# Optimization experiments

Hardware: AMD Instinct MI355X
Metric: run time of the kernel (lower is better)

The kernel has to match this reference:

```python
import jax, jax.numpy as jnp
import numpy as np

B = 32          # num graphs
N = 4096        # nodes per graph (temporal length after reshape)
TOT = B * N     # 131072 total nodes
F = 64          # num_features
HS = 128        # hidden_dim_s
RS = 32         # rank_s
HT = 128        # hidden_dim_t
RT = 32         # rank_t
E = 1048576     # num edges


def setup_inputs() -> dict:
    key = jax.random.key(0)
    ks = jax.random.split(key, 20)
    x = jax.random.normal(ks[0], (TOT, F), jnp.float32)
    edge_index = jax.random.randint(ks[1], (2, E), 0, TOT, dtype=jnp.int64)
    batch = jnp.repeat(jnp.arange(B, dtype=jnp.int64), N)

    def lin(k, fan_in, fan_out):
        s = 1.0 / np.sqrt(fan_in)
        return jax.random.uniform(k, (fan_in, fan_out), jnp.float32, -s, s)

    def conv(k, cout, cin):
        s = 1.0 / np.sqrt(cin * 3)
        return jax.random.uniform(k, (cout, cin, 3), jnp.float32, -s, s)

    return {
        "x": x, "edge_index": edge_index, "batch": batch,
        "W1": lin(ks[2], F, HS), "b1": jnp.zeros((HS,), jnp.float32),
        "W2": lin(ks[3], HS, RS), "b2": jnp.zeros((RS,), jnp.float32),
        "W3": lin(ks[4], RS, HS), "b3": jnp.zeros((HS,), jnp.float32),
        "tW1": conv(ks[5], HT, HS), "tb1": jnp.zeros((HT,), jnp.float32),
        "tW2": conv(ks[6], RT, HT), "tb2": jnp.zeros((RT,), jnp.float32),
        "tW3": conv(ks[7], HT, RT), "tb3": jnp.zeros((HT,), jnp.float32),
        "Wpi": lin(ks[8], HT, 1), "bpi": jnp.zeros((1,), jnp.float32),
        "Wn": lin(ks[9], HT, 1), "bn": jnp.zeros((1,), jnp.float32),
        "Wp": lin(ks[10], HT, 1), "bp": jnp.zeros((1,), jnp.float32),
    }


def reference(x, edge_index, batch,
              W1, b1, W2, b2, W3, b3,
              tW1, tb1, tW2, tb2, tW3, tb3,
              Wpi, bpi, Wn, bn, Wp, bp):
    src, dst = edge_index[0], edge_index[1]
    n = x.shape[0]

    # GCN symmetric normalization with added self-loops (PyG GCNConv default)
    deg = jnp.zeros((n,), x.dtype).at[dst].add(1.0) + 1.0  # +1 self-loop
    dinv = jax.lax.rsqrt(deg)
    enorm = dinv[src] * dinv[dst]       # [E] edge normalization
    snorm = dinv * dinv                 # [n] self-loop normalization

    def gcn(h, W, b):
        h = h @ W                                            # [n, out]
        agg = jnp.zeros_like(h).at[dst].add(h[src] * enorm[:, None])
        return agg + h * snorm[:, None] + b

    xs = jax.nn.relu(gcn(x, W1, b1))
    xs = jax.nn.relu(gcn(xs, W2, b2))
    xs = jax.nn.relu(gcn(xs, W3, b3))    # [TOT, HS]

    num_graphs = B  # == batch.max() + 1 (batch is repeat(arange(B), N))
    xs = xs.reshape(num_graphs, -1, xs.shape[-1]).transpose(0, 2, 1)  # [B, HS, N]

    def conv1d(z, w, bias):
        y = jax.lax.conv_general_dilated(
            z, w, window_strides=(1,), padding=((1, 1),),
            dimension_numbers=("NCH", "OIH", "NCH"))
        return y + bias[None, :, None]

    xt = jax.nn.relu(conv1d(xs, tW1, tb1))
    xt = jax.nn.relu(conv1d(xt, tW2, tb2))
    xt = jax.nn.relu(conv1d(xt, tW3, tb3))                   # [B, HT, N]

    xt = xt.transpose(0, 2, 1).reshape(-1, xt.shape[1])      # [TOT, HT]

    pi = jax.nn.sigmoid(xt @ Wpi + bpi)
    nb = jax.nn.softplus(xt @ Wn + bn)
    p = jax.nn.sigmoid(xt @ Wp + bp)
    return (pi, nb, p)
```

## Files before the change

kernel.cpp:

```cpp
#include <hip/hip_runtime.h>
#include <cmath>

constexpr int TOT = 131072;
constexpr int NE  = 1048576;
constexpr int NMASK = 4095;

constexpr int NB   = 512;
constexpr int DPB  = 256;
constexpr int BCAP = 4096;
constexpr int EPB  = 2048;

typedef __attribute__((ext_vector_type(8))) short bf16x8;
typedef __attribute__((ext_vector_type(4))) float f32x4;

__device__ inline float bf2f(unsigned int u16) {
    union { unsigned int i; float f; } x; x.i = u16 << 16; return x.f;
}
__device__ inline unsigned short f2bf(float f) {
    union { float f; unsigned int i; } x; x.f = f;
    unsigned int r = (x.i + 0x7fffu + ((x.i >> 16) & 1u)) >> 16;
    return (unsigned short)r;
}
__device__ inline void unpack8(uint4 v, float* f) {
    f[0] = bf2f(v.x & 0xffffu); f[1] = bf2f(v.x >> 16);
    f[2] = bf2f(v.y & 0xffffu); f[3] = bf2f(v.y >> 16);
    f[4] = bf2f(v.z & 0xffffu); f[5] = bf2f(v.z >> 16);
    f[6] = bf2f(v.w & 0xffffu); f[7] = bf2f(v.w >> 16);
}
__device__ inline uint4 pack8(const float* f) {
    uint4 v;
    v.x = (unsigned)f2bf(f[0]) | ((unsigned)f2bf(f[1]) << 16);
    v.y = (unsigned)f2bf(f[2]) | ((unsigned)f2bf(f[3]) << 16);
    v.z = (unsigned)f2bf(f[4]) | ((unsigned)f2bf(f[5]) << 16);
    v.w = (unsigned)f2bf(f[6]) | ((unsigned)f2bf(f[7]) << 16);
    return v;
}

__global__ __launch_bounds__(256) void k_part(const int* __restrict__ src,
                                              const int* __restrict__ dst,
                                              int* __restrict__ gcur,
                                              unsigned* __restrict__ buf) {
    __shared__ int hist[NB];
    __shared__ int cbase[NB];
    __shared__ int lcur[NB];
    const int tid = threadIdx.x;
    const int e0 = blockIdx.x * EPB;

    for (int b = tid; b < NB; b += 256) hist[b] = 0;
    __syncthreads();
    for (int i = tid; i < EPB; i += 256)
        atomicAdd(&hist[dst[e0 + i] >> 8], 1);
    __syncthreads();
    for (int b = tid; b < NB; b += 256) {
        int c = hist[b];
        cbase[b] = (c > 0) ? atomicAdd(&gcur[b * 32], c) : 0;
        lcur[b] = 0;
    }
    __syncthreads();
    for (int i = tid; i < EPB; i += 256) {
        int e = e0 + i;
        int d = dst[e];
        int b = d >> 8;
        int p = atomicAdd(&lcur[b], 1);
        buf[b * BCAP + cbase[b] + p] = ((unsigned)src[e] << 8) | (unsigned)(d & 255);
    }
}

__global__ __launch_bounds__(256) void k_bcsr(const unsigned* __restrict__ buf,
                                              const int* __restrict__ gcur,
                                              int* __restrict__ adj,
                                              int2* __restrict__ rse,
                                              float* __restrict__ dinv,
                                              const float4* __restrict__ x,
                                              uint4* __restrict__ xsc) {
    __shared__ int cnt[DPB];
    __shared__ int start[DPB];
    __shared__ int cur[DPB];
    __shared__ int sc[DPB];
    const int b = blockIdx.x;
    const int tid = threadIdx.x;
    cnt[tid] = 0;
    __syncthreads();
    const int n = gcur[b * 32];
    const unsigned* eb = buf + b * BCAP;
    for (int i = tid; i < n; i += 256)
        atomicAdd(&cnt[eb[i] & 255u], 1);
    __syncthreads();
    int v = cnt[tid];
    sc[tid] = v;
    __syncthreads();
    for (int off = 1; off < 256; off <<= 1) {
        int a = sc[tid];
        int p = (tid >= off) ? sc[tid - off] : 0;
        __syncthreads();
        sc[tid] = a + p;
        __syncthreads();
    }
    int st = sc[tid] - v;
    start[tid] = st;
    cur[tid] = 0;
    int d = (b << 8) + tid;
    rse[d] = make_int2(b * BCAP + st, v);
    dinv[d] = rsqrtf((float)v + 1.0f);
    __syncthreads();
    for (int i = tid; i < n; i += 256) {
        unsigned w = eb[i];
        int dl = (int)(w & 255u);
        int p = atomicAdd(&cur[dl], 1);
        adj[b * BCAP + start[dl] + p] = (int)(w >> 8);
    }
    for (int i = tid; i < DPB * 8; i += 256) {
        int rl = i >> 3;
        int t = (b << 11) + i;
        float dv = rsqrtf((float)cnt[rl] + 1.0f);
        float4 v0 = x[t * 2], v1 = x[t * 2 + 1];
        float f[8] = { v0.x * dv, v0.y * dv, v0.z * dv, v0.w * dv,
                       v1.x * dv, v1.y * dv, v1.z * dv, v1.w * dv };
        xsc[t] = pack8(f);
    }
}

__global__ __launch_bounds__(256) void k_packall(
    const float* __restrict__ W1, const float* __restrict__ W2, const float* __restrict__ W3,
    const float* __restrict__ tW1, const float* __restrict__ tW2, const float* __restrict__ tW3,
    unsigned short* __restrict__ g1, unsigned short* __restrict__ g2, unsigned short* __restrict__ g3,
    unsigned short* __restrict__ c1, unsigned short* __restrict__ c2, unsigned short* __restrict__ c3) {
    int gid = blockIdx.x * 256 + threadIdx.x;
    const float* w; unsigned short* wp; int CIN, COUT, taps, idx;
    if      (gid <  8192) { w = W1;  wp = g1; CIN = 64;  COUT = 128; taps = 1; idx = gid; }
    else if (gid < 12288) { w = W2;  wp = g2; CIN = 128; COUT = 32;  taps = 1; idx = gid - 8192; }
    else if (gid < 16384) { w = W3;  wp = g3; CIN = 32;  COUT = 128; taps = 1; idx = gid - 12288; }
    else if (gid < 65536) { w = tW1; wp = c1; CIN = 128; COUT = 128; taps = 3; idx = gid - 16384; }
    else if (gid < 77824) { w = tW2; wp = c2; CIN = 128; COUT = 32;  taps = 3; idx = gid - 65536; }
    else if (gid < 90112) { w = tW3; wp = c3; CIN = 32;  COUT = 128; taps = 3; idx = gid - 77824; }
    else return;
    int j = idx & 7;
    int L = (idx >> 3) & 63;
    int f = idx >> 9;
    int NT = COUT >> 4;
    int kc = f / NT, nt = f - kc * NT;
    int k = kc * 32 + (L >> 4) * 8 + j;
    int n = nt * 16 + (L & 15);
    float v;
    if (taps == 1) v = w[k * COUT + n];
    else { int t = k / CIN, c = k - t * CIN; v = w[(n * CIN + c) * 3 + t]; }
    wp[idx] = f2bf(v);
}

template<int LC>
__global__ __launch_bounds__(256) void k_gcsr(const uint4* __restrict__ xs,
                                              const int* __restrict__ adj,
                                              const int2* __restrict__ rse,
                                              const float* __restrict__ dinv,
                                              const float* __restrict__ bias,
                                              uint4* __restrict__ out) {
    int t = blockIdx.x * 256 + threadIdx.x;
    int d = t >> LC;
    int g = t & ((1 << LC) - 1);
    float a[8];
    unpack8(xs[t], a);
    int2 se = rse[d];
    int e = se.x, end = se.x + se.y;
    for (; e + 4 <= end; e += 4) {
        int s0 = adj[e], s1 = adj[e + 1], s2 = adj[e + 2], s3 = adj[e + 3];
        uint4 v0 = xs[(s0 << LC) + g];
        uint4 v1 = xs[(s1 << LC) + g];
        uint4 v2 = xs[(s2 << LC) + g];
        uint4 v3 = xs[(s3 << LC) + g];
        float f[8];
        unpack8(v0, f);
#pragma unroll
        for (int j = 0; j < 8; ++j) a[j] += f[j];
        unpack8(v1, f);
#pragma unroll
        for (int j = 0; j < 8; ++j) a[j] += f[j];
        unpack8(v2, f);
#pragma unroll
        for (int j = 0; j < 8; ++j) a[j] += f[j];
        unpack8(v3, f);
#pragma unroll
        for (int j = 0; j < 8; ++j) a[j] += f[j];
    }
    for (; e < end; ++e) {
        float f[8];
        unpack8(xs[(adj[e] << LC) + g], f);
#pragma unroll
        for (int j = 0; j < 8; ++j) a[j] += f[j];
    }
    float dv = dinv[d];
#pragma unroll
    for (int j = 0; j < 8; ++j)
        a[j] = fmaxf(fmaf(a[j], dv, bias[g * 8 + j]), 0.0f) * dv;
    out[t] = pack8(a);
}

template<int CIN, bool RELU>
__global__ __launch_bounds__(256) void k_gmm(const uint4* __restrict__ xs,
                                             const int* __restrict__ adj,
                                             const int2* __restrict__ rse,
                                             const float* __restrict__ dinv,
                                             const bf16x8* __restrict__ wp,
                                             const float* __restrict__ bias,
                                             unsigned short* __restrict__ y) {
    constexpr int COUT = 128;
    constexpr int ROWS = 64;
    constexpr int SC = CIN + 8;
    constexpr int NV = CIN / 8;
    constexpr int VPT = NV / 4;
    constexpr int NK = CIN / 32;
    constexpr int NT = COUT / 16;
    constexpr int WN = 2, WM = 4;
    __shared__ __attribute__((aligned(16))) unsigned short tile[ROWS * SC];

    const int R0 = blockIdx.x * ROWS;
    const int tid = threadIdx.x;

    {
        int r = R0 + (tid >> 2);
        int g = tid & 3;
        const uint4* base = xs + (long)r * NV + g * VPT;
        float a[VPT * 8];
#pragma unroll
        for (int v = 0; v < VPT; ++v) unpack8(base[v], a + v * 8);
        int2 se = rse[r];
        int e = se.x, end = se.x + se.y;
        for (; e + 4 <= end; e += 4) {
            int s0 = adj[e], s1 = adj[e + 1], s2 = adj[e + 2], s3 = adj[e + 3];
            const uint4* p0 = xs + (long)s0 * NV + g * VPT;
            const uint4* p1 = xs + (long)s1 * NV + g * VPT;
            const uint4* p2 = xs + (long)s2 * NV + g * VPT;
            const uint4* p3 = xs + (long)s3 * NV + g * VPT;
            uint4 v0[VPT], v1[VPT], v2[VPT], v3[VPT];
#pragma unroll
            for (int v = 0; v < VPT; ++v) { v0[v] = p0[v]; v1[v] = p1[v]; v2[v] = p2[v]; v3[v] = p3[v]; }
            float f[VPT * 8];
#pragma unroll
            for (int v = 0; v < VPT; ++v) unpack8(v0[v], f + v * 8);
#pragma unroll
            for (int j = 0; j < VPT * 8; ++j) a[j] += f[j];
#pragma unroll
            for (int v = 0; v < VPT; ++v) unpack8(v1[v], f + v * 8);
#pragma unroll
            for (int j = 0; j < VPT * 8; ++j) a[j] += f[j];
#pragma unroll
            for (int v = 0; v < VPT; ++v) unpack8(v2[v], f + v * 8);
#pragma unroll
            for (int j = 0; j < VPT * 8; ++j) a[j] += f[j];
#pragma unroll
            for (int v = 0; v < VPT; ++v) unpack8(v3[v], f + v * 8);
#pragma unroll
            for (int j = 0; j < VPT * 8; ++j) a[j] += f[j];
        }
        for (; e < end; ++e) {
            const uint4* p0 = xs + (long)adj[e] * NV + g * VPT;
            float f[VPT * 8];
#pragma unroll
            for (int v = 0; v < VPT; ++v) unpack8(p0[v], f + v * 8);
#pragma unroll
            for (int j = 0; j < VPT * 8; ++j) a[j] += f[j];
        }
        float dv = dinv[r];
#pragma unroll
        for (int j = 0; j < VPT * 8; ++j) a[j] *= dv;
        uint4* dst4 = (uint4*)(tile + (tid >> 2) * SC + g * VPT * 8);
#pragma unroll
        for (int v = 0; v < VPT; ++v) dst4[v] = pack8(a + v * 8);
    }
    __syncthreads();

    const int lane = threadIdx.x & 63;
    const int w = threadIdx.x >> 6;
    const int l16 = lane & 15;
    const int q = lane >> 4;
    const int colbase = w * 32;
    const int nt0 = colbase >> 4;

    f32x4 acc[WM][WN];
#pragma unroll
    for (int wm = 0; wm < WM; ++wm)
#pragma unroll
        for (int nt = 0; nt < WN; ++nt) acc[wm][nt] = (f32x4){0.f, 0.f, 0.f, 0.f};

    const bf16x8* __restrict__ wpl = wp + lane;

#pragma unroll
    for (int kc = 0; kc < NK; ++kc) {
        bf16x8 a[WM];
#pragma unroll
        for (int wm = 0; wm < WM; ++wm)
            a[wm] = *(const bf16x8*)(tile + (wm * 16 + l16) * SC + kc * 32 + q * 8);
        bf16x8 b[WN];
#pragma unroll
        for (int nt = 0; nt < WN; ++nt)
            b[nt] = wpl[(kc * NT + nt0 + nt) * 64];
#pragma unroll
        for (int wm = 0; wm < WM; ++wm)
#pragma unroll
            for (int nt = 0; nt < WN; ++nt)
                acc[wm][nt] = __builtin_amdgcn_mfma_f32_16x16x32_bf16(a[wm], b[nt], acc[wm][nt], 0, 0, 0);
    }

#pragma unroll
    for (int wm = 0; wm < WM; ++wm) {
#pragma unroll
        for (int nt = 0; nt < WN; ++nt) {
            int col = colbase + nt * 16 + l16;
            float bi = bias[col];
#pragma unroll
            for (int r = 0; r < 4; ++r) {
                int row = R0 + wm * 16 + q * 4 + r;
                float v = acc[wm][nt][r] + bi;
                if (RELU) v = fmaxf(v, 0.0f);
                y[(long)row * COUT + col] = f2bf(v);
            }
        }
    }
}

template<int CIN, int COUT, bool SOUT>
__global__ __launch_bounds__(256) void k_mm(const unsigned short* __restrict__ x,
                                            const bf16x8* __restrict__ wp,
                                            const float* __restrict__ dinv,
                                            unsigned short* __restrict__ y) {
    constexpr int ROWS = 64;
    constexpr int SC = CIN + 8;
    constexpr int NK = CIN / 32;
    constexpr int NT = COUT / 16;
    constexpr int WN = 1, WM = 2;
    __shared__ __attribute__((aligned(16))) unsigned short tile[ROWS * SC];

    const int R0 = blockIdx.x * ROWS;

    constexpr int NLD = ROWS * (CIN / 8);
    for (int idx = threadIdx.x; idx < NLD; idx += 256) {
        int tr = idx / (CIN / 8);
        int c8 = idx - tr * (CIN / 8);
        uint4 v = *(const uint4*)(x + (long)(R0 + tr) * CIN + c8 * 8);
        *(uint4*)(tile + tr * SC + c8 * 8) = v;
    }
    __syncthreads();

    const int lane = threadIdx.x & 63;
    const int w = threadIdx.x >> 6;
    const int l16 = lane & 15;
    const int q = lane >> 4;
    const int colbase = (w & 1) * 16;
    const int rowbase = (w >> 1) * 32;
    const int nt0 = colbase >> 4;

    f32x4 acc[WM][WN];
#pragma unroll
    for (int wm = 0; wm < WM; ++wm)
#pragma unroll
        for (int nt = 0; nt < WN; ++nt) acc[wm][nt] = (f32x4){0.f, 0.f, 0.f, 0.f};

    const bf16x8* __restrict__ wpl = wp + lane;

#pragma unroll
    for (int kc = 0; kc < NK; ++kc) {
        bf16x8 a[WM];
#pragma unroll
        for (int wm = 0; wm < WM; ++wm)
            a[wm] = *(const bf16x8*)(tile + (rowbase + wm * 16 + l16) * SC + kc * 32 + q * 8);
        bf16x8 b[WN];
#pragma unroll
        for (int nt = 0; nt < WN; ++nt)
            b[nt] = wpl[(kc * NT + nt0 + nt) * 64];
#pragma unroll
        for (int wm = 0; wm < WM; ++wm)
#pragma unroll
            for (int nt = 0; nt < WN; ++nt)
                acc[wm][nt] = __builtin_amdgcn_mfma_f32_16x16x32_bf16(a[wm], b[nt], acc[wm][nt], 0, 0, 0);
    }

#pragma unroll
    for (int wm = 0; wm < WM; ++wm) {
#pragma unroll
        for (int nt = 0; nt < WN; ++nt) {
            int col = colbase + nt * 16 + l16;
#pragma unroll
            for (int r = 0; r < 4; ++r) {
                int row = R0 + rowbase + wm * 16 + q * 4 + r;
                float v = acc[wm][nt][r];
                if (SOUT) v *= dinv[row];
                y[(long)row * COUT + col] = f2bf(v);
            }
        }
    }
}

__global__ __launch_bounds__(256) void k_tconv_heads(
    const unsigned short* __restrict__ x,
    const bf16x8* __restrict__ wp1, const float* __restrict__ tb1,
    const bf16x8* __restrict__ wp2, const float* __restrict__ tb2,
    const bf16x8* __restrict__ wp3, const float* __restrict__ tb3,
    const float* __restrict__ Wpi, const float* __restrict__ bpi,
    const float* __restrict__ Wn,  const float* __restrict__ bn,
    const float* __restrict__ Wp,  const float* __restrict__ bp,
    float* __restrict__ out) {
    constexpr int SC1 = 136;
    constexpr int SC2 = 40;
    __shared__ __attribute__((aligned(16))) unsigned short shl[82 * 136 * 2 + 66 * 40];
    unsigned short* xin = shl;
    unsigned short* c1  = shl + 82 * 136;
    unsigned short* c2  = shl + 2 * 82 * 136;
    unsigned short* xts = shl;

    const int R0 = blockIdx.x * 64;
    const int n0 = R0 & NMASK;
    const int tid = threadIdx.x;

    for (int i = tid; i < 82 * 16; i += 256) {
        int r = i >> 4;
        int c8 = i & 15;
        int n = n0 - 3 + r;
        uint4 v = make_uint4(0, 0, 0, 0);
        if (n >= 0 && n < 4096)
            v = *(const uint4*)(x + (long)(R0 - 3 + r) * 128 + c8 * 8);
        *(uint4*)(xin + r * SC1 + c8 * 8) = v;
    }
    for (int i = tid; i < 2 * 16; i += 256)
        *(uint4*)(c1 + (80 + (i >> 4)) * SC1 + (i & 15) * 8) = make_uint4(0, 0, 0, 0);
    __syncthreads();

    const int lane = tid & 63;
    const int w = tid >> 6;
    const int l16 = lane & 15;
    const int q = lane >> 4;

    {
        f32x4 acc[5][2];
#pragma unroll
        for (int rt = 0; rt < 5; ++rt)
#pragma unroll
            for (int nt = 0; nt < 2; ++nt) acc[rt][nt] = (f32x4){0.f, 0.f, 0.f, 0.f};
        const bf16x8* wpl = wp1 + lane;
#pragma unroll
        for (int kc = 0; kc < 12; ++kc) {
            int tap = kc >> 2, ch = kc & 3;
            bf16x8 a[5];
#pragma unroll
            for (int rt = 0; rt < 5; ++rt)
                a[rt] = *(const bf16x8*)(xin + (16 * rt + l16 + tap) * SC1 + ch * 32 + q * 8);
            bf16x8 b[2];
#pragma unroll
            for (int nt = 0; nt < 2; ++nt)
                b[nt] = wpl[(kc * 8 + 2 * w + nt) * 64];
#pragma unroll
            for (int rt = 0; rt < 5; ++rt)
#pragma unroll
                for (int nt = 0; nt < 2; ++nt)
                    acc[rt][nt] = __builtin_amdgcn_mfma_f32_16x16x32_bf16(a[rt], b[nt], acc[rt][nt], 0, 0, 0);
        }
#pragma unroll
        for (int rt = 0; rt < 5; ++rt) {
#pragma unroll
            for (int nt = 0; nt < 2; ++nt) {
                int col = w * 32 + nt * 16 + l16;
                float bi = tb1[col];
#pragma unroll
                for (int r = 0; r < 4; ++r) {
                    int idx = 16 * rt + q * 4 + r;
                    int n = n0 - 2 + idx;
                    unsigned short v = 0;
                    if (n >= 0 && n < 4096)
                        v = f2bf(fmaxf(acc[rt][nt][r] + bi, 0.0f));
                    c1[idx * SC1 + col] = v;
                }
            }
        }
    }
    __syncthreads();

    for (int rt = w; rt < 5; rt += 4) {
        f32x4 acc[2];
#pragma unroll
        for (int nt = 0; nt < 2; ++nt) acc[nt] = (f32x4){0.f, 0.f, 0.f, 0.f};
        const bf16x8* wpl = wp2 + lane;
#pragma unroll
        for (int kc = 0; kc < 12; ++kc) {
            int tap = kc >> 2, ch = kc & 3;
            bf16x8 a = *(const bf16x8*)(c1 + (16 * rt + l16 + tap) * SC1 + ch * 32 + q * 8);
            bf16x8 b0 = wpl[(kc * 2 + 0) * 64];
            bf16x8 b1 = wpl[(kc * 2 + 1) * 64];
            acc[0] = __builtin_amdgcn_mfma_f32_16x16x32_bf16(a, b0, acc[0], 0, 0, 0);
            acc[1] = __builtin_amdgcn_mfma_f32_16x16x32_bf16(a, b1, acc[1], 0, 0, 0);
        }
#pragma unroll
        for (int nt = 0; nt < 2; ++nt) {
            int col = nt * 16 + l16;
            float bi = tb2[col];
#pragma unroll
            for (int r = 0; r < 4; ++r) {
                int idx = 16 * rt + q * 4 + r;
                if (idx < 66) {
                    int n = n0 - 1 + idx;
                    unsigned short v = 0;
                    if (n >= 0 && n < 4096)
                        v = f2bf(fmaxf(acc[nt][r] + bi, 0.0f));
                    c2[idx * SC2 + col] = v;
                }
            }
        }
    }
    __syncthreads();

    {
        f32x4 acc[4][2];
#pragma unroll
        for (int rt = 0; rt < 4; ++rt)
#pragma unroll
            for (int nt = 0; nt < 2; ++nt) acc[rt][nt] = (f32x4){0.f, 0.f, 0.f, 0.f};
        const bf16x8* wpl = wp3 + lane;
#pragma unroll
        for (int kc = 0; kc < 3; ++kc) {
            bf16x8 a[4];
#pragma unroll
            for (int rt = 0; rt < 4; ++rt)
                a[rt] = *(const bf16x8*)(c2 + (16 * rt + l16 + kc) * SC2 + q * 8);
            bf16x8 b[2];
#pragma unroll
            for (int nt = 0; nt < 2; ++nt)
                b[nt] = wpl[(kc * 8 + 2 * w + nt) * 64];
#pragma unroll
            for (int rt = 0; rt < 4; ++rt)
#pragma unroll
                for (int nt = 0; nt < 2; ++nt)
                    acc[rt][nt] = __builtin_amdgcn_mfma_f32_16x16x32_bf16(a[rt], b[nt], acc[rt][nt], 0, 0, 0);
        }
        __syncthreads();
#pragma unroll
        for (int rt = 0; rt < 4; ++rt) {
#pragma unroll
            for (int nt = 0; nt < 2; ++nt) {
                int col = w * 32 + nt * 16 + l16;
                float bi = tb3[col];
#pragma unroll
                for (int r = 0; r < 4; ++r) {
                    int row = 16 * rt + q * 4 + r;
                    xts[row * 130 + col] = f2bf(fmaxf(acc[rt][nt][r] + bi, 0.0f));
                }
            }
        }
    }
    __syncthreads();

    if (tid < 192) {
        int h = tid >> 6;
        int row = tid & 63;
        const float* Wh = (h == 0) ? Wpi : (h == 1) ? Wn : Wp;
        float s = 0.0f;
        const unsigned short* xr = xts + row * 130;
#pragma unroll
        for (int c2i = 0; c2i < 64; ++c2i) {
            unsigned u = *(const unsigned*)(xr + c2i * 2);
            s = fmaf(bf2f(u & 0xffffu), Wh[c2i * 2], s);
            s = fmaf(bf2f(u >> 16), Wh[c2i * 2 + 1], s);
        }
        float bb = (h == 0) ? bpi[0] : (h == 1) ? bn[0] : bp[0];
        float z = s + bb;
        float o;
        if (h == 1) o = (z > 20.0f) ? z : log1pf(expf(z));
        else        o = 1.0f / (1.0f + expf(-z));
        out[h * TOT + R0 + row] = o;
    }
}

extern "C" void kernel_launch(void* const* d_in, const int* in_sizes, int n_in,
                              void* d_out, int out_size, void* d_ws, size_t ws_size,
                              hipStream_t stream) {
    const float* x   = (const float*)d_in[0];
    const int*   ei  = (const int*)d_in[1];
    const int*   src = ei;
    const int*   dst = ei + NE;
    const float* W1 = (const float*)d_in[3];
    const float* b1 = (const float*)d_in[4];
    const float* W2 = (const float*)d_in[5];
    const float* b2 = (const float*)d_in[6];
    const float* W3 = (const float*)d_in[7];
    const float* b3 = (const float*)d_in[8];
    const float* tW1 = (const float*)d_in[9];
    const float* tb1 = (const float*)d_in[10];
    const float* tW2 = (const float*)d_in[11];
    const float* tb2 = (const float*)d_in[12];
    const float* tW3 = (const float*)d_in[13];
    const float* tb3 = (const float*)d_in[14];
    const float* Wpi = (const float*)d_in[15];
    const float* bpi = (const float*)d_in[16];
    const float* Wn  = (const float*)d_in[17];
    const float* bn  = (const float*)d_in[18];
    const float* Wp  = (const float*)d_in[19];
    const float* bp  = (const float*)d_in[20];

    char* ws = (char*)d_ws;
    float* dinv = (float*)(ws + (0ull << 20));
    int*   gcur = (int*)  (ws + (1ull << 20));
    int2*  rse  = (int2*) (ws + (1ull << 20) + (256 << 10));
    unsigned short* wpG1 = (unsigned short*)(ws + (3ull << 20));
    unsigned short* wpG2 = (unsigned short*)(ws + (3ull << 20) + (128 << 10));
    unsigned short* wpG3 = (unsigned short*)(ws + (3ull << 20) + (256 << 10));
    unsigned short* wpC1 = (unsigned short*)(ws + (3ull << 20) + (384 << 10));
    unsigned short* wpC2 = (unsigned short*)(ws + (3ull << 20) + (512 << 10));
    unsigned short* wpC3 = (unsigned short*)(ws + (3ull << 20) + (640 << 10));
    unsigned* buf = (unsigned*)(ws + (4ull << 20));
    int* adj = (int*)(ws + (12ull << 20));
    unsigned short* Xa = (unsigned short*)(ws + (24ull  << 20));
    unsigned short* Xb = (unsigned short*)(ws + (44ull  << 20));
    unsigned short* Xc = (unsigned short*)(ws + (80ull  << 20));
    unsigned short* Xd = (unsigned short*)(ws + (116ull << 20));
    unsigned short* Xe = (unsigned short*)(ws + (128ull << 20));

    hipMemsetAsync(gcur, 0, NB * 32 * sizeof(int), stream);
    k_packall<<<352, 256, 0, stream>>>(W1, W2, W3, tW1, tW2, tW3,
                                       wpG1, wpG2, wpG3, wpC1, wpC2, wpC3);

    k_part<<<NE / EPB, 256, 0, stream>>>(src, dst, gcur, buf);
    k_bcsr<<<NB, 256, 0, stream>>>(buf, gcur, adj, rse, dinv, (const float4*)x, (uint4*)Xa);

    k_gmm<64, true><<<TOT / 64, 256, 0, stream>>>((const uint4*)Xa, adj, rse, dinv,
                                                  (const bf16x8*)wpG1, b1, Xc);

    k_mm<128, 32, true><<<TOT / 64, 256, 0, stream>>>(Xc, (const bf16x8*)wpG2, dinv, Xd);
    k_gcsr<2><<<TOT * 4 / 256, 256, 0, stream>>>((const uint4*)Xd, adj, rse, dinv,
                                                 b2, (uint4*)Xe);

    k_gmm<32, true><<<TOT / 64, 256, 0, stream>>>((const uint4*)Xe, adj, rse, dinv,
                                                  (const bf16x8*)wpG3, b3, Xb);

    k_tconv_heads<<<TOT / 64, 256, 0, stream>>>(Xb,
                                                (const bf16x8*)wpC1, tb1,
                                                (const bf16x8*)wpC2, tb2,
                                                (const bf16x8*)wpC3, tb3,
                                                Wpi, bpi, Wn, bn, Wp, bp, (float*)d_out);
}
```

Baseline: 288.0 us.

## Split first temporal conv into separate kernel and fold weight packing into partition

The first 128->128 temporal conv moves out of the fused tconv+heads kernel into a generalized k_mm kernel with tap/halo support, bias and ReLU. The fused kernel now only does conv2, conv3 and the heads, which cuts its LDS footprint and should raise occupancy, and it no longer recomputes halo rows for conv1. Weight packing is merged into k_part, saving one launch. In exchange, conv1's output now takes an extra round trip through global memory.

```diff
diff --git a/kernel.cpp b/kernel.cpp
--- a/kernel.cpp
+++ b/kernel.cpp
@@ -36,10 +36,30 @@
     return v;
 }
 
+__device__ inline void pack_one(const float* __restrict__ w, unsigned short* __restrict__ wp,
+                                int CIN, int COUT, int taps, int idx) {
+    int j = idx & 7;
+    int L = (idx >> 3) & 63;
+    int f = idx >> 9;
+    int NT = COUT >> 4;
+    int kc = f / NT, nt = f - kc * NT;
+    int k = kc * 32 + (L >> 4) * 8 + j;
+    int n = nt * 16 + (L & 15);
+    float v;
+    if (taps == 1) v = w[k * COUT + n];
+    else { int t = k / CIN, c = k - t * CIN; v = w[(n * CIN + c) * 3 + t]; }
+    wp[idx] = f2bf(v);
+}
+
+struct PackArgs {
+    const float *W1, *W2, *W3, *tW1, *tW2, *tW3;
+    unsigned short *g1, *g2, *g3, *c1, *c2, *c3;
+};
 __global__ __launch_bounds__(256) void k_part(const int* __restrict__ src,
                                               const int* __restrict__ dst,
                                               int* __restrict__ gcur,
-                                              unsigned* __restrict__ buf) {
+                                              unsigned* __restrict__ buf,
+                                              PackArgs pa) {
     __shared__ int hist[NB];
     __shared__ int cbase[NB];
     __shared__ int lcur[NB];
@@ -64,6 +84,13 @@
         int p = atomicAdd(&lcur[b], 1);
         buf[b * BCAP + cbase[b] + p] = ((unsigned)src[e] << 8) | (unsigned)(d & 255);
     }
+    int gid = blockIdx.x * 256 + tid;
+    if      (gid <  8192) pack_one(pa.W1,  pa.g1, 64, 128, 1, gid);
+    else if (gid < 12288) pack_one(pa.W2,  pa.g2, 128, 32, 1, gid - 8192);
+    else if (gid < 16384) pack_one(pa.W3,  pa.g3, 32, 128, 1, gid - 12288);
+    else if (gid < 65536) pack_one(pa.tW1, pa.c1, 128, 128, 3, gid - 16384);
+    else if (gid < 77824) pack_one(pa.tW2, pa.c2, 128, 32, 3, gid - 65536);
+    else if (gid < 90112) pack_one(pa.tW3, pa.c3, 32, 128, 3, gid - 77824);
 }
 
 __global__ __launch_bounds__(256) void k_bcsr(const unsigned* __restrict__ buf,
@@ -118,33 +145,6 @@
                        v1.x * dv, v1.y * dv, v1.z * dv, v1.w * dv };
         xsc[t] = pack8(f);
     }
-}
-
-__global__ __launch_bounds__(256) void k_packall(
-    const float* __restrict__ W1, const float* __restrict__ W2, const float* __restrict__ W3,
-    const float* __restrict__ tW1, const float* __restrict__ tW2, const float* __restrict__ tW3,
-    unsigned short* __restrict__ g1, unsigned short* __restrict__ g2, unsigned short* __restrict__ g3,
-    unsigned short* __restrict__ c1, unsigned short* __restrict__ c2, unsigned short* __restrict__ c3) {
-    int gid = blockIdx.x * 256 + threadIdx.x;
-    const float* w; unsigned short* wp; int CIN, COUT, taps, idx;
-    if      (gid <  8192) { w = W1;  wp = g1; CIN = 64;  COUT = 128; taps = 1; idx = gid; }
-    else if (gid < 12288) { w = W2;  wp = g2; CIN = 128; COUT = 32;  taps = 1; idx = gid - 8192; }
-    else if (gid < 16384) { w = W3;  wp = g3; CIN = 32;  COUT = 128; taps = 1; idx = gid - 12288; }
-    else if (gid < 65536) { w = tW1; wp = c1; CIN = 128; COUT = 128; taps = 3; idx = gid - 16384; }
-    else if (gid < 77824) { w = tW2; wp = c2; CIN = 128; COUT = 32;  taps = 3; idx = gid - 65536; }
-    else if (gid < 90112) { w = tW3; wp = c3; CIN = 32;  COUT = 128; taps = 3; idx = gid - 77824; }
-    else return;
-    int j = idx & 7;
-    int L = (idx >> 3) & 63;
-    int f = idx >> 9;
-    int NT = COUT >> 4;
-    int kc = f / NT, nt = f - kc * NT;
-    int k = kc * 32 + (L >> 4) * 8 + j;
-    int n = nt * 16 + (L & 15);
-    float v;
-    if (taps == 1) v = w[k * COUT + n];
-    else { int t = k / CIN, c = k - t * CIN; v = w[(n * CIN + c) * 3 + t]; }
-    wp[idx] = f2bf(v);
 }
 
 template<int LC>
@@ -317,25 +317,38 @@
     }
 }
 
-template<int CIN, int COUT, bool SOUT>
+template<int CIN, int COUT, int TAPS, bool RELU, bool BIAS, bool SOUT>
 __global__ __launch_bounds__(256) void k_mm(const unsigned short* __restrict__ x,
                                             const bf16x8* __restrict__ wp,
+                                            const float* __restrict__ bias,
                                             const float* __restrict__ dinv,
                                             unsigned short* __restrict__ y) {
     constexpr int ROWS = 64;
+    constexpr int HALO = (TAPS == 3) ? 1 : 0;
+    constexpr int TR = ROWS + 2 * HALO;
     constexpr int SC = CIN + 8;
-    constexpr int NK = CIN / 32;
+    constexpr int NCH = CIN / 32;
+    constexpr int NK = TAPS * NCH;
     constexpr int NT = COUT / 16;
-    constexpr int WN = 1, WM = 2;
-    __shared__ __attribute__((aligned(16))) unsigned short tile[ROWS * SC];
+    constexpr int WN = (COUT == 128) ? 2 : 1;
+    constexpr int WM = (COUT == 128) ? 4 : 2;
+    __shared__ __attribute__((aligned(16))) unsigned short tile[TR * SC];
 
     const int R0 = blockIdx.x * ROWS;
-
-    constexpr int NLD = ROWS * (CIN / 8);
+    const int n0 = R0 & NMASK; (void)n0;
+
+    constexpr int NLD = TR * (CIN / 8);
     for (int idx = threadIdx.x; idx < NLD; idx += 256) {
         int tr = idx / (CIN / 8);
         int c8 = idx - tr * (CIN / 8);
-        uint4 v = *(const uint4*)(x + (long)(R0 + tr) * CIN + c8 * 8);
+        int ro = tr - HALO;
+        bool valid = true;
+        if (TAPS == 3) {
+            if (ro < 0) valid = (n0 > 0);
+            else if (ro >= ROWS) valid = (n0 + ROWS < 4096);
+        }
+        uint4 v = make_uint4(0, 0, 0, 0);
+        if (valid) v = *(const uint4*)(x + (long)(R0 + ro) * CIN + c8 * 8);
         *(uint4*)(tile + tr * SC + c8 * 8) = v;
     }
     __syncthreads();
@@ -344,8 +357,8 @@
     const int w = threadIdx.x >> 6;
     const int l16 = lane & 15;
     const int q = lane >> 4;
-    const int colbase = (w & 1) * 16;
-    const int rowbase = (w >> 1) * 32;
+    const int colbase = (COUT == 128) ? w * 32 : (w & 1) * 16;
+    const int rowbase = (COUT == 128) ? 0 : (w >> 1) * 32;
     const int nt0 = colbase >> 4;
 
     f32x4 acc[WM][WN];
@@ -358,10 +371,12 @@
 
 #pragma unroll
     for (int kc = 0; kc < NK; ++kc) {
+        const int tap = (TAPS == 3) ? (kc / NCH) : 0;
+        const int ch  = (TAPS == 3) ? (kc - tap * NCH) : kc;
         bf16x8 a[WM];
 #pragma unroll
         for (int wm = 0; wm < WM; ++wm)
-            a[wm] = *(const bf16x8*)(tile + (rowbase + wm * 16 + l16) * SC + kc * 32 + q * 8);
+            a[wm] = *(const bf16x8*)(tile + (rowbase + wm * 16 + l16 + tap) * SC + ch * 32 + q * 8);
         bf16x8 b[WN];
 #pragma unroll
         for (int nt = 0; nt < WN; ++nt)
@@ -378,10 +393,12 @@
 #pragma unroll
         for (int nt = 0; nt < WN; ++nt) {
             int col = colbase + nt * 16 + l16;
+            float bi = BIAS ? bias[col] : 0.0f;
 #pragma unroll
             for (int r = 0; r < 4; ++r) {
                 int row = R0 + rowbase + wm * 16 + q * 4 + r;
-                float v = acc[wm][nt][r];
+                float v = acc[wm][nt][r] + bi;
+                if (RELU) v = fmaxf(v, 0.0f);
                 if (SOUT) v *= dinv[row];
                 y[(long)row * COUT + col] = f2bf(v);
             }
@@ -389,9 +406,8 @@
     }
 }
 
-__global__ __launch_bounds__(256) void k_tconv_heads(
+__global__ __launch_bounds__(256) void k_c23_heads(
     const unsigned short* __restrict__ x,
-    const bf16x8* __restrict__ wp1, const float* __restrict__ tb1,
     const bf16x8* __restrict__ wp2, const float* __restrict__ tb2,
     const bf16x8* __restrict__ wp3, const float* __restrict__ tb3,
     const float* __restrict__ Wpi, const float* __restrict__ bpi,
@@ -400,10 +416,9 @@
     float* __restrict__ out) {
     constexpr int SC1 = 136;
     constexpr int SC2 = 40;
-    __shared__ __attribute__((aligned(16))) unsigned short shl[82 * 136 * 2 + 66 * 40];
-    unsigned short* xin = shl;
-    unsigned short* c1  = shl + 82 * 136;
-    unsigned short* c2  = shl + 2 * 82 * 136;
+    __shared__ __attribute__((aligned(16))) unsigned short shl[82 * 136 + 66 * 40];
+    unsigned short* c1  = shl;
+    unsigned short* c2  = shl + 82 * 136;
     unsigned short* xts = shl;
 
     const int R0 = blockIdx.x * 64;
@@ -413,64 +428,18 @@
     for (int i = tid; i < 82 * 16; i += 256) {
         int r = i >> 4;
         int c8 = i & 15;
-        int n = n0 - 3 + r;
+        int n = n0 - 2 + r;
         uint4 v = make_uint4(0, 0, 0, 0);
         if (n >= 0 && n < 4096)
-            v = *(const uint4*)(x + (long)(R0 - 3 + r) * 128 + c8 * 8);
-        *(uint4*)(xin + r * SC1 + c8 * 8) = v;
-    }
-    for (int i = tid; i < 2 * 16; i += 256)
-        *(uint4*)(c1 + (80 + (i >> 4)) * SC1 + (i & 15) * 8) = make_uint4(0, 0, 0, 0);
+            v = *(const uint4*)(x + (long)(R0 - 2 + r) * 128 + c8 * 8);
+        *(uint4*)(c1 + r * SC1 + c8 * 8) = v;
+    }
     __syncthreads();
 
     const int lane = tid & 63;
     const int w = tid >> 6;
     const int l16 = lane & 15;
     const int q = lane >> 4;
-
-    {
-        f32x4 acc[5][2];
-#pragma unroll
-        for (int rt = 0; rt < 5; ++rt)
-#pragma unroll
-            for (int nt = 0; nt < 2; ++nt) acc[rt][nt] = (f32x4){0.f, 0.f, 0.f, 0.f};
-        const bf16x8* wpl = wp1 + lane;
-#pragma unroll
-        for (int kc = 0; kc < 12; ++kc) {
-            int tap = kc >> 2, ch = kc & 3;
-            bf16x8 a[5];
-#pragma unroll
-            for (int rt = 0; rt < 5; ++rt)
-                a[rt] = *(const bf16x8*)(xin + (16 * rt + l16 + tap) * SC1 + ch * 32 + q * 8);
-            bf16x8 b[2];
-#pragma unroll
-            for (int nt = 0; nt < 2; ++nt)
-                b[nt] = wpl[(kc * 8 + 2 * w + nt) * 64];
-#pragma unroll
-            for (int rt = 0; rt < 5; ++rt)
-#pragma unroll
-                for (int nt = 0; nt < 2; ++nt)
-                    acc[rt][nt] = __builtin_amdgcn_mfma_f32_16x16x32_bf16(a[rt], b[nt], acc[rt][nt], 0, 0, 0);
-        }
-#pragma unroll
-        for (int rt = 0; rt < 5; ++rt) {
-#pragma unroll
-            for (int nt = 0; nt < 2; ++nt) {
-                int col = w * 32 + nt * 16 + l16;
-                float bi = tb1[col];
-#pragma unroll
-                for (int r = 0; r < 4; ++r) {
-                    int idx = 16 * rt + q * 4 + r;
-                    int n = n0 - 2 + idx;
-                    unsigned short v = 0;
-                    if (n >= 0 && n < 4096)
-                        v = f2bf(fmaxf(acc[rt][nt][r] + bi, 0.0f));
-                    c1[idx * SC1 + col] = v;
-                }
-            }
-        }
-    }
-    __syncthreads();
 
     for (int rt = w; rt < 5; rt += 4) {
         f32x4 acc[2];
@@ -528,7 +497,6 @@
                 for (int nt = 0; nt < 2; ++nt)
                     acc[rt][nt] = __builtin_amdgcn_mfma_f32_16x16x32_bf16(a[rt], b[nt], acc[rt][nt], 0, 0, 0);
         }
-        __syncthreads();
 #pragma unroll
         for (int rt = 0; rt < 4; ++rt) {
 #pragma unroll
@@ -611,25 +579,27 @@
     unsigned short* Xe = (unsigned short*)(ws + (128ull << 20));
 
     hipMemsetAsync(gcur, 0, NB * 32 * sizeof(int), stream);
-    k_packall<<<352, 256, 0, stream>>>(W1, W2, W3, tW1, tW2, tW3,
-                                       wpG1, wpG2, wpG3, wpC1, wpC2, wpC3);
-
-    k_part<<<NE / EPB, 256, 0, stream>>>(src, dst, gcur, buf);
+
+    PackArgs pa = { W1, W2, W3, tW1, tW2, tW3, wpG1, wpG2, wpG3, wpC1, wpC2, wpC3 };
+    k_part<<<NE / EPB, 256, 0, stream>>>(src, dst, gcur, buf, pa);
     k_bcsr<<<NB, 256, 0, stream>>>(buf, gcur, adj, rse, dinv, (const float4*)x, (uint4*)Xa);
 
     k_gmm<64, true><<<TOT / 64, 256, 0, stream>>>((const uint4*)Xa, adj, rse, dinv,
                                                   (const bf16x8*)wpG1, b1, Xc);
 
-    k_mm<128, 32, true><<<TOT / 64, 256, 0, stream>>>(Xc, (const bf16x8*)wpG2, dinv, Xd);
+    k_mm<128, 32, 1, false, false, true>
+        <<<TOT / 64, 256, 0, stream>>>(Xc, (const bf16x8*)wpG2, nullptr, dinv, Xd);
     k_gcsr<2><<<TOT * 4 / 256, 256, 0, stream>>>((const uint4*)Xd, adj, rse, dinv,
                                                  b2, (uint4*)Xe);
 
     k_gmm<32, true><<<TOT / 64, 256, 0, stream>>>((const uint4*)Xe, adj, rse, dinv,
                                                   (const bf16x8*)wpG3, b3, Xb);
 
-    k_tconv_heads<<<TOT / 64, 256, 0, stream>>>(Xb,
-                                                (const bf16x8*)wpC1, tb1,
-                                                (const bf16x8*)wpC2, tb2,
-                                                (const bf16x8*)wpC3, tb3,
-                                                Wpi, bpi, Wn, bn, Wp, bp, (float*)d_out);
-}
+    k_mm<128, 128, 3, true, true, false>
+        <<<TOT / 64, 256, 0, stream>>>(Xb, (const bf16x8*)wpC1, tb1, nullptr, Xc);
+
+    k_c23_heads<<<TOT / 64, 256, 0, stream>>>(Xc,
+                                              (const bf16x8*)wpC2, tb2,
+                                              (const bf16x8*)wpC3, tb3,
+                                              Wpi, bpi, Wn, bn, Wp, bp, (float*)d_out);
+}
```

Result: no change. 287.3 us (-0.2%).
